# Performance work log

Hardware: AMD Instinct MI355X
Metric: run time of the kernel (lower is better)

The kernel has to match this reference:

```python
import jax, jax.numpy as jnp
import numpy as np

LN_EPS = 1e-5
BN_EPS = 1e-5


def setup_inputs() -> dict:
    key = jax.random.key(0)
    ks = jax.random.split(key, 16)
    N, C, T, H, W = 4, 256, 5, 28, 28
    Ci = 128
    CA = 128  # audio feature dim (hard-coded 128 in nn.Linear(128, in_channels))
    s = 0.02
    inp = {
        "x": jax.random.normal(ks[0], (N, C, T, H, W), jnp.float32),
        "audio": jax.random.normal(ks[1], (N, T, CA), jnp.float32),
        "align_W": jax.random.normal(ks[2], (C, CA), jnp.float32) * s,
        "align_b": jax.random.normal(ks[3], (C,), jnp.float32) * s,
        "g_W": jax.random.normal(ks[4], (Ci, C), jnp.float32) * s,
        "g_b": jax.random.normal(ks[5], (Ci,), jnp.float32) * s,
        "theta_W": jax.random.normal(ks[6], (Ci, C), jnp.float32) * s,
        "theta_b": jax.random.normal(ks[7], (Ci,), jnp.float32) * s,
        "phi_W": jax.random.normal(ks[8], (Ci, C), jnp.float32) * s,
        "phi_b": jax.random.normal(ks[9], (Ci,), jnp.float32) * s,
        "Wz_W": jax.random.normal(ks[10], (C, Ci), jnp.float32) * s,
        "Wz_b": jax.random.normal(ks[11], (C,), jnp.float32) * s,
        "bn_gamma": jax.random.normal(ks[12], (C,), jnp.float32) * s + 1.0,
        "bn_beta": jax.random.normal(ks[13], (C,), jnp.float32) * s,
        "bn_mean": jnp.zeros((C,), jnp.float32),
        "bn_var": jnp.ones((C,), jnp.float32),
        "ln_gamma": jnp.ones((C,), jnp.float32),
        "ln_beta": jnp.zeros((C,), jnp.float32),
    }
    return inp


def _tpavi(x, audio, align_W, align_b, g_W, g_b, theta_W, theta_b,
           phi_W, phi_b, Wz_W, Wz_b, bn_gamma, bn_beta, bn_mean, bn_var,
           ln_gamma, ln_beta):
    N, C, T, H, W = x.shape
    L = T * H * W
    # audio alignment: Linear(128 -> C), then broadcast over H, W
    audio_temp = jnp.einsum('ntc,oc->nto', audio, align_W) + align_b     # (N,T,C)
    a = audio_temp.transpose(0, 2, 1)[:, :, :, None, None]               # (N,C,T,1,1)
    a = jnp.broadcast_to(a, (N, C, T, H, W)).reshape(N, C, L)            # (N,C,L)

    xf = x.reshape(N, C, L)                                              # (N,C,L)
    # 1x1 conv3d == per-token channel mixing
    g_x = jnp.einsum('oc,ncl->nlo', g_W, xf) + g_b                       # (N,L,Ci)
    theta_x = jnp.einsum('oc,ncl->nlo', theta_W, xf) + theta_b           # (N,L,Ci)
    phi_x = jnp.einsum('oc,ncl->nol', phi_W, a) + phi_b[None, :, None]   # (N,Ci,L)

    # dot mode: f = theta phi^T, normalized by token count (no softmax)
    f = jnp.einsum('nlo,nok->nlk', theta_x, phi_x)                       # (N,L,L)
    f_div_C = f / L
    y = jnp.einsum('nlk,nko->nlo', f_div_C, g_x)                         # (N,L,Ci)

    y = y.transpose(0, 2, 1)                                             # (N,Ci,L)
    # W_z: 1x1 conv (Ci -> C) + BatchNorm3d (inference statistics)
    wy = jnp.einsum('oc,ncl->nol', Wz_W, y) + Wz_b[None, :, None]        # (N,C,L)
    inv = bn_gamma / jnp.sqrt(bn_var + BN_EPS)
    wy = (wy - bn_mean[None, :, None]) * inv[None, :, None] + bn_beta[None, :, None]

    z = wy.reshape(N, C, T, H, W) + x                                    # residual
    # LayerNorm over channel dim (channels-last in the original)
    zt = z.transpose(0, 2, 3, 4, 1)                                      # (N,T,H,W,C)
    mu = jnp.mean(zt, axis=-1, keepdims=True)
    var = jnp.mean(jnp.square(zt - mu), axis=-1, keepdims=True)
    zt = (zt - mu) / jnp.sqrt(var + LN_EPS) * ln_gamma + ln_beta
    z = zt.transpose(0, 4, 1, 2, 3)                                      # (N,C,T,H,W)
    return z, audio_temp


def reference(x, audio, align_W, align_b, g_W, g_b, theta_W, theta_b,
              phi_W, phi_b, Wz_W, Wz_b, bn_gamma, bn_beta, bn_mean, bn_var,
              ln_gamma, ln_beta):
    return _tpavi(x, audio, align_W, align_b, g_W, g_b, theta_W, theta_b,
                  phi_W, phi_b, Wz_W, Wz_b, bn_gamma, bn_beta, bn_mean, bn_var,
                  ln_gamma, ln_beta)
```

## Files before the change

### kernel.cpp

```cpp
#include <hip/hip_runtime.h>

#define N_DIM 4
#define C_DIM 256
#define T_DIM 5
#define HW    784
#define L_TOK 3920
#define CI    128
#define CA    128

#define WS_XS  0
#define WS_TP  5120
#define WS_GW  10240
#define WS_TB  15360

__global__ __launch_bounds__(256) void k1_xsum(const float* __restrict__ x,
                                               float* __restrict__ ws) {
    int bid = blockIdx.x;
    int n   = bid / (C_DIM * T_DIM);
    int rem = bid % (C_DIM * T_DIM);
    int c   = rem / T_DIM;
    int t   = rem % T_DIM;
    const float* base = x + ((size_t)(n * C_DIM + c) * T_DIM + t) * HW;
    int tid = threadIdx.x;

    float p = base[tid] + base[tid + 256] + base[tid + 512];
    if (tid < HW - 768) p += base[tid + 768];

    for (int off = 32; off > 0; off >>= 1) p += __shfl_down(p, off, 64);
    __shared__ float wsum[4];
    if ((tid & 63) == 0) wsum[tid >> 6] = p;
    __syncthreads();
    if (tid == 0) {
        ws[WS_XS + (n * T_DIM + t) * C_DIM + c] = wsum[0] + wsum[1] + wsum[2] + wsum[3];
    }
}

__global__ __launch_bounds__(256) void k2_small(
    const float* __restrict__ audio,   const float* __restrict__ align_W,
    const float* __restrict__ align_b, const float* __restrict__ g_W,
    const float* __restrict__ g_b,     const float* __restrict__ theta_W,
    const float* __restrict__ theta_b, const float* __restrict__ phi_W,
    const float* __restrict__ phi_b,   const float* __restrict__ Wz_W,
    const float* __restrict__ bn_gamma,const float* __restrict__ bn_var,
    float* __restrict__ ws, float* __restrict__ out_audio) {
    int nt = blockIdx.x;
    int tid = threadIdx.x;

    __shared__ float at_s[C_DIM];
    __shared__ float xs_s[C_DIM];
    __shared__ float phi_s[CI];
    __shared__ float g_s[CI];

    {
        const float* arow = audio + nt * CA;
        const float* wrow = align_W + tid * CA;
        float acc = align_b[tid];
        for (int a = 0; a < CA; ++a) acc = fmaf(arow[a], wrow[a], acc);
        at_s[tid] = acc;
        out_audio[nt * C_DIM + tid] = acc;
    }
    xs_s[tid] = ws[WS_XS + nt * C_DIM + tid];
    __syncthreads();

    if (tid < CI) {
        float acc = phi_b[tid];
        const float* wrow = phi_W + tid * C_DIM;
        for (int c = 0; c < C_DIM; ++c) acc = fmaf(wrow[c], at_s[c], acc);
        phi_s[tid] = acc;
        float ga = (float)HW * g_b[tid];
        const float* grow = g_W + tid * C_DIM;
        for (int c = 0; c < C_DIM; ++c) ga = fmaf(grow[c], xs_s[c], ga);
        g_s[tid] = ga;
    }
    __syncthreads();

    {
        float acc = 0.f;
        for (int o = 0; o < CI; ++o) acc = fmaf(theta_W[o * C_DIM + tid], phi_s[o], acc);
        ws[WS_TP + nt * C_DIM + tid] = acc;
    }
    if (tid == 0) {
        float acc = 0.f;
        for (int o = 0; o < CI; ++o) acc = fmaf(theta_b[o], phi_s[o], acc);
        ws[WS_TB + nt] = acc;
    }
    {
        float acc = 0.f;
        const float* wr = Wz_W + tid * CI;
        for (int o = 0; o < CI; ++o) acc = fmaf(wr[o], g_s[o], acc);
        float inv = bn_gamma[tid] * rsqrtf(bn_var[tid] + 1e-5f);
        ws[WS_GW + nt * C_DIM + tid] = acc * inv * (1.0f / (float)L_TOK);
    }
}

__global__ __launch_bounds__(256) void k3_main(
    const float* __restrict__ x,        const float* __restrict__ ws,
    const float* __restrict__ Wz_b,     const float* __restrict__ bn_gamma,
    const float* __restrict__ bn_beta,  const float* __restrict__ bn_mean,
    const float* __restrict__ bn_var,   const float* __restrict__ ln_gamma,
    const float* __restrict__ ln_beta,  float* __restrict__ out) {
    __shared__ float TPs[T_DIM * C_DIM];
    __shared__ float GWs[T_DIM * C_DIM];
    __shared__ float tb_s[T_DIM];
    __shared__ float B_s[C_DIM], lng_s[C_DIM], lnb_s[C_DIM];
    __shared__ float zbuf[64 * 257];
    __shared__ float Fp[256 * 5];
    __shared__ float Sp[256 * 2];

    int n    = blockIdx.y;
    int tile = blockIdx.x;
    int tid  = threadIdx.x;
    int g    = tid >> 6;
    int li   = tid & 63;
    int l    = tile * 64 + li;
    bool act = (l < L_TOK);

    for (int i = tid; i < T_DIM * C_DIM; i += 256) {
        TPs[i] = ws[WS_TP + n * T_DIM * C_DIM + i];
        GWs[i] = ws[WS_GW + n * T_DIM * C_DIM + i];
    }
    if (tid < T_DIM) tb_s[tid] = ws[WS_TB + n * T_DIM + tid];
    {
        int c = tid;
        float inv = bn_gamma[c] * rsqrtf(bn_var[c] + 1e-5f);
        B_s[c]   = (Wz_b[c] - bn_mean[c]) * inv + bn_beta[c];
        lng_s[c] = ln_gamma[c];
        lnb_s[c] = ln_beta[c];
    }
    __syncthreads();

    float F0 = 0, F1 = 0, F2 = 0, F3 = 0, F4 = 0;
    const float* xb = x + ((size_t)n * C_DIM + g * 64) * L_TOK + l;
    float* zrow = zbuf + li * 257 + g * 64;
    if (act) {
        for (int j = 0; j < 64; ++j) {
            float xv = xb[j * L_TOK];
            zrow[j] = xv;
            const float* tp = TPs + g * 64 + j;
            F0 = fmaf(xv, tp[0],    F0);
            F1 = fmaf(xv, tp[256],  F1);
            F2 = fmaf(xv, tp[512],  F2);
            F3 = fmaf(xv, tp[768],  F3);
            F4 = fmaf(xv, tp[1024], F4);
        }
    }
    Fp[tid * 5 + 0] = F0; Fp[tid * 5 + 1] = F1; Fp[tid * 5 + 2] = F2;
    Fp[tid * 5 + 3] = F3; Fp[tid * 5 + 4] = F4;
    __syncthreads();

    float Ft[T_DIM];
    #pragma unroll
    for (int t = 0; t < T_DIM; ++t)
        Ft[t] = Fp[(0 * 64 + li) * 5 + t] + Fp[(1 * 64 + li) * 5 + t] +
                Fp[(2 * 64 + li) * 5 + t] + Fp[(3 * 64 + li) * 5 + t] + tb_s[t];
    float s1 = 0.f, s2 = 0.f;
    for (int j = 0; j < 64; ++j) {
        int c = g * 64 + j;
        float zc = B_s[c] + zrow[j];
        zc = fmaf(Ft[0], GWs[c],        zc);
        zc = fmaf(Ft[1], GWs[256 + c],  zc);
        zc = fmaf(Ft[2], GWs[512 + c],  zc);
        zc = fmaf(Ft[3], GWs[768 + c],  zc);
        zc = fmaf(Ft[4], GWs[1024 + c], zc);
        zrow[j] = zc;
        s1 += zc;
        s2 = fmaf(zc, zc, s2);
    }
    Sp[tid * 2]     = s1;
    Sp[tid * 2 + 1] = s2;
    __syncthreads();

    float t1 = Sp[li * 2]     + Sp[(64 + li) * 2]     + Sp[(128 + li) * 2]     + Sp[(192 + li) * 2];
    float t2 = Sp[li * 2 + 1] + Sp[(64 + li) * 2 + 1] + Sp[(128 + li) * 2 + 1] + Sp[(192 + li) * 2 + 1];
    float mu   = t1 * (1.0f / C_DIM);
    float var  = t2 * (1.0f / C_DIM) - mu * mu;
    float rstd = rsqrtf(var + 1e-5f);
    if (act) {
        float* ob = out + ((size_t)n * C_DIM + g * 64) * L_TOK + l;
        for (int j = 0; j < 64; ++j) {
            int c = g * 64 + j;
            float zc = zrow[j];
            ob[j * L_TOK] = fmaf((zc - mu) * rstd, lng_s[c], lnb_s[c]);
        }
    }
}

extern "C" void kernel_launch(void* const* d_in, const int* in_sizes, int n_in,
                              void* d_out, int out_size, void* d_ws, size_t ws_size,
                              hipStream_t stream) {
    const float* x        = (const float*)d_in[0];
    const float* audio    = (const float*)d_in[1];
    const float* align_W  = (const float*)d_in[2];
    const float* align_b  = (const float*)d_in[3];
    const float* g_W      = (const float*)d_in[4];
    const float* g_b      = (const float*)d_in[5];
    const float* theta_W  = (const float*)d_in[6];
    const float* theta_b  = (const float*)d_in[7];
    const float* phi_W    = (const float*)d_in[8];
    const float* phi_b    = (const float*)d_in[9];
    const float* Wz_W     = (const float*)d_in[10];
    const float* Wz_b     = (const float*)d_in[11];
    const float* bn_gamma = (const float*)d_in[12];
    const float* bn_beta  = (const float*)d_in[13];
    const float* bn_mean  = (const float*)d_in[14];
    const float* bn_var   = (const float*)d_in[15];
    const float* ln_gamma = (const float*)d_in[16];
    const float* ln_beta  = (const float*)d_in[17];

    float* out       = (float*)d_out;
    float* out_audio = out + (size_t)N_DIM * C_DIM * L_TOK;
    float* ws        = (float*)d_ws;

    k1_xsum<<<N_DIM * C_DIM * T_DIM, 256, 0, stream>>>(x, ws);
    k2_small<<<N_DIM * T_DIM, 256, 0, stream>>>(
        audio, align_W, align_b, g_W, g_b, theta_W, theta_b, phi_W, phi_b,
        Wz_W, bn_gamma, bn_var, ws, out_audio);
    dim3 grid3((L_TOK + 63) / 64, N_DIM);
    k3_main<<<grid3, 256, 0, stream>>>(
        x, ws, Wz_b, bn_gamma, bn_beta, bn_mean, bn_var, ln_gamma, ln_beta, out);
}
```

Baseline: 138.6 us.

## Hold per-token channels in registers with 1024-thread blocks in main kernel

The main kernel now uses 1024 threads per block, with each wave covering 16 channels instead of 64. Each thread keeps its x values in registers, which removes the large shared-memory z buffer and the strided LDS traffic it caused. The partial-sum reductions widen to 16 waves. The x-sum and small projection kernels also switch to float4 loads with split accumulators, and the theta-bias dot product becomes a wave shuffle reduction. The gain in memory-level parallelism per token comes at the cost of heavier block-wide reductions and a larger block size.

```diff
diff --git a/kernel.cpp b/kernel.cpp
--- a/kernel.cpp
+++ b/kernel.cpp
@@ -20,12 +20,14 @@
     int rem = bid % (C_DIM * T_DIM);
     int c   = rem / T_DIM;
     int t   = rem % T_DIM;
-    const float* base = x + ((size_t)(n * C_DIM + c) * T_DIM + t) * HW;
+    const float4* base = (const float4*)(x + ((size_t)(n * C_DIM + c) * T_DIM + t) * HW);
     int tid = threadIdx.x;
 
-    float p = base[tid] + base[tid + 256] + base[tid + 512];
-    if (tid < HW - 768) p += base[tid + 768];
-
+    float p = 0.f;
+    if (tid < HW / 4) {
+        float4 v = base[tid];
+        p = (v.x + v.y) + (v.z + v.w);
+    }
     for (int off = 32; off > 0; off >>= 1) p += __shfl_down(p, off, 64);
     __shared__ float wsum[4];
     if ((tid & 63) == 0) wsum[tid >> 6] = p;
@@ -46,54 +48,89 @@
     int nt = blockIdx.x;
     int tid = threadIdx.x;
 
+    __shared__ float audio_s[CA];
     __shared__ float at_s[C_DIM];
     __shared__ float xs_s[C_DIM];
     __shared__ float phi_s[CI];
     __shared__ float g_s[CI];
 
+    if (tid < CA) audio_s[tid] = audio[nt * CA + tid];
+    xs_s[tid] = ws[WS_XS + nt * C_DIM + tid];
+    __syncthreads();
+
     {
-        const float* arow = audio + nt * CA;
-        const float* wrow = align_W + tid * CA;
-        float acc = align_b[tid];
-        for (int a = 0; a < CA; ++a) acc = fmaf(arow[a], wrow[a], acc);
+        const float4* row = (const float4*)(align_W + tid * CA);
+        float a0 = 0, a1 = 0, a2 = 0, a3 = 0;
+        #pragma unroll
+        for (int k = 0; k < CA / 4; ++k) {
+            float4 w = row[k];
+            a0 = fmaf(w.x, audio_s[4 * k + 0], a0);
+            a1 = fmaf(w.y, audio_s[4 * k + 1], a1);
+            a2 = fmaf(w.z, audio_s[4 * k + 2], a2);
+            a3 = fmaf(w.w, audio_s[4 * k + 3], a3);
+        }
+        float acc = align_b[tid] + (a0 + a1) + (a2 + a3);
         at_s[tid] = acc;
         out_audio[nt * C_DIM + tid] = acc;
     }
-    xs_s[tid] = ws[WS_XS + nt * C_DIM + tid];
     __syncthreads();
 
     if (tid < CI) {
-        float acc = phi_b[tid];
-        const float* wrow = phi_W + tid * C_DIM;
-        for (int c = 0; c < C_DIM; ++c) acc = fmaf(wrow[c], at_s[c], acc);
-        phi_s[tid] = acc;
-        float ga = (float)HW * g_b[tid];
-        const float* grow = g_W + tid * C_DIM;
-        for (int c = 0; c < C_DIM; ++c) ga = fmaf(grow[c], xs_s[c], ga);
-        g_s[tid] = ga;
+        const float4* prow = (const float4*)(phi_W + tid * C_DIM);
+        const float4* grow = (const float4*)(g_W + tid * C_DIM);
+        float p0 = 0, p1 = 0, p2 = 0, p3 = 0;
+        float q0 = 0, q1 = 0, q2 = 0, q3 = 0;
+        #pragma unroll
+        for (int k = 0; k < C_DIM / 4; ++k) {
+            float4 w = prow[k];
+            float4 u = grow[k];
+            float b0 = at_s[4 * k + 0], b1 = at_s[4 * k + 1];
+            float b2 = at_s[4 * k + 2], b3 = at_s[4 * k + 3];
+            float c0 = xs_s[4 * k + 0], c1 = xs_s[4 * k + 1];
+            float c2 = xs_s[4 * k + 2], c3 = xs_s[4 * k + 3];
+            p0 = fmaf(w.x, b0, p0); p1 = fmaf(w.y, b1, p1);
+            p2 = fmaf(w.z, b2, p2); p3 = fmaf(w.w, b3, p3);
+            q0 = fmaf(u.x, c0, q0); q1 = fmaf(u.y, c1, q1);
+            q2 = fmaf(u.z, c2, q2); q3 = fmaf(u.w, c3, q3);
+        }
+        phi_s[tid] = phi_b[tid] + (p0 + p1) + (p2 + p3);
+        g_s[tid]   = (float)HW * g_b[tid] + (q0 + q1) + (q2 + q3);
     }
     __syncthreads();
 
     {
-        float acc = 0.f;
-        for (int o = 0; o < CI; ++o) acc = fmaf(theta_W[o * C_DIM + tid], phi_s[o], acc);
-        ws[WS_TP + nt * C_DIM + tid] = acc;
-    }
-    if (tid == 0) {
-        float acc = 0.f;
-        for (int o = 0; o < CI; ++o) acc = fmaf(theta_b[o], phi_s[o], acc);
-        ws[WS_TB + nt] = acc;
+        float a0 = 0, a1 = 0, a2 = 0, a3 = 0;
+        #pragma unroll 4
+        for (int o = 0; o < CI; o += 4) {
+            a0 = fmaf(theta_W[(o + 0) * C_DIM + tid], phi_s[o + 0], a0);
+            a1 = fmaf(theta_W[(o + 1) * C_DIM + tid], phi_s[o + 1], a1);
+            a2 = fmaf(theta_W[(o + 2) * C_DIM + tid], phi_s[o + 2], a2);
+            a3 = fmaf(theta_W[(o + 3) * C_DIM + tid], phi_s[o + 3], a3);
+        }
+        ws[WS_TP + nt * C_DIM + tid] = (a0 + a1) + (a2 + a3);
+    }
+    if (tid < 64) {
+        float p = theta_b[tid] * phi_s[tid] + theta_b[tid + 64] * phi_s[tid + 64];
+        for (int off = 32; off > 0; off >>= 1) p += __shfl_down(p, off, 64);
+        if (tid == 0) ws[WS_TB + nt] = p;
     }
     {
-        float acc = 0.f;
-        const float* wr = Wz_W + tid * CI;
-        for (int o = 0; o < CI; ++o) acc = fmaf(wr[o], g_s[o], acc);
+        const float4* row = (const float4*)(Wz_W + tid * CI);
+        float a0 = 0, a1 = 0, a2 = 0, a3 = 0;
+        #pragma unroll
+        for (int k = 0; k < CI / 4; ++k) {
+            float4 w = row[k];
+            a0 = fmaf(w.x, g_s[4 * k + 0], a0);
+            a1 = fmaf(w.y, g_s[4 * k + 1], a1);
+            a2 = fmaf(w.z, g_s[4 * k + 2], a2);
+            a3 = fmaf(w.w, g_s[4 * k + 3], a3);
+        }
         float inv = bn_gamma[tid] * rsqrtf(bn_var[tid] + 1e-5f);
-        ws[WS_GW + nt * C_DIM + tid] = acc * inv * (1.0f / (float)L_TOK);
-    }
-}
-
-__global__ __launch_bounds__(256) void k3_main(
+        ws[WS_GW + nt * C_DIM + tid] = ((a0 + a1) + (a2 + a3)) * inv * (1.0f / (float)L_TOK);
+    }
+}
+
+__global__ __launch_bounds__(1024) void k3_main(
     const float* __restrict__ x,        const float* __restrict__ ws,
     const float* __restrict__ Wz_b,     const float* __restrict__ bn_gamma,
     const float* __restrict__ bn_beta,  const float* __restrict__ bn_mean,
@@ -103,9 +140,8 @@
     __shared__ float GWs[T_DIM * C_DIM];
     __shared__ float tb_s[T_DIM];
     __shared__ float B_s[C_DIM], lng_s[C_DIM], lnb_s[C_DIM];
-    __shared__ float zbuf[64 * 257];
-    __shared__ float Fp[256 * 5];
-    __shared__ float Sp[256 * 2];
+    __shared__ float Fp[T_DIM * 1024];
+    __shared__ float Sp[2 * 1024];
 
     int n    = blockIdx.y;
     int tile = blockIdx.x;
@@ -115,12 +151,12 @@
     int l    = tile * 64 + li;
     bool act = (l < L_TOK);
 
-    for (int i = tid; i < T_DIM * C_DIM; i += 256) {
+    for (int i = tid; i < T_DIM * C_DIM; i += 1024) {
         TPs[i] = ws[WS_TP + n * T_DIM * C_DIM + i];
         GWs[i] = ws[WS_GW + n * T_DIM * C_DIM + i];
     }
     if (tid < T_DIM) tb_s[tid] = ws[WS_TB + n * T_DIM + tid];
-    {
+    if (tid < C_DIM) {
         int c = tid;
         float inv = bn_gamma[c] * rsqrtf(bn_var[c] + 1e-5f);
         B_s[c]   = (Wz_b[c] - bn_mean[c]) * inv + bn_beta[c];
@@ -129,58 +165,66 @@
     }
     __syncthreads();
 
+    float xz[16];
+    const float* xb = x + ((size_t)(n * C_DIM + g * 16)) * L_TOK + l;
+    #pragma unroll
+    for (int j = 0; j < 16; ++j) xz[j] = act ? xb[(size_t)j * L_TOK] : 0.f;
+
     float F0 = 0, F1 = 0, F2 = 0, F3 = 0, F4 = 0;
-    const float* xb = x + ((size_t)n * C_DIM + g * 64) * L_TOK + l;
-    float* zrow = zbuf + li * 257 + g * 64;
-    if (act) {
-        for (int j = 0; j < 64; ++j) {
-            float xv = xb[j * L_TOK];
-            zrow[j] = xv;
-            const float* tp = TPs + g * 64 + j;
-            F0 = fmaf(xv, tp[0],    F0);
-            F1 = fmaf(xv, tp[256],  F1);
-            F2 = fmaf(xv, tp[512],  F2);
-            F3 = fmaf(xv, tp[768],  F3);
-            F4 = fmaf(xv, tp[1024], F4);
-        }
-    }
-    Fp[tid * 5 + 0] = F0; Fp[tid * 5 + 1] = F1; Fp[tid * 5 + 2] = F2;
-    Fp[tid * 5 + 3] = F3; Fp[tid * 5 + 4] = F4;
+    #pragma unroll
+    for (int j = 0; j < 16; ++j) {
+        const float* tp = TPs + g * 16 + j;
+        F0 = fmaf(xz[j], tp[0],    F0);
+        F1 = fmaf(xz[j], tp[256],  F1);
+        F2 = fmaf(xz[j], tp[512],  F2);
+        F3 = fmaf(xz[j], tp[768],  F3);
+        F4 = fmaf(xz[j], tp[1024], F4);
+    }
+    Fp[0 * 1024 + tid] = F0; Fp[1 * 1024 + tid] = F1; Fp[2 * 1024 + tid] = F2;
+    Fp[3 * 1024 + tid] = F3; Fp[4 * 1024 + tid] = F4;
     __syncthreads();
 
     float Ft[T_DIM];
     #pragma unroll
-    for (int t = 0; t < T_DIM; ++t)
-        Ft[t] = Fp[(0 * 64 + li) * 5 + t] + Fp[(1 * 64 + li) * 5 + t] +
-                Fp[(2 * 64 + li) * 5 + t] + Fp[(3 * 64 + li) * 5 + t] + tb_s[t];
+    for (int t = 0; t < T_DIM; ++t) {
+        float a = tb_s[t];
+        #pragma unroll
+        for (int w = 0; w < 16; ++w) a += Fp[t * 1024 + w * 64 + li];
+        Ft[t] = a;
+    }
     float s1 = 0.f, s2 = 0.f;
-    for (int j = 0; j < 64; ++j) {
-        int c = g * 64 + j;
-        float zc = B_s[c] + zrow[j];
+    #pragma unroll
+    for (int j = 0; j < 16; ++j) {
+        int c = g * 16 + j;
+        float zc = B_s[c] + xz[j];
         zc = fmaf(Ft[0], GWs[c],        zc);
         zc = fmaf(Ft[1], GWs[256 + c],  zc);
         zc = fmaf(Ft[2], GWs[512 + c],  zc);
         zc = fmaf(Ft[3], GWs[768 + c],  zc);
         zc = fmaf(Ft[4], GWs[1024 + c], zc);
-        zrow[j] = zc;
+        xz[j] = zc;
         s1 += zc;
         s2 = fmaf(zc, zc, s2);
     }
-    Sp[tid * 2]     = s1;
-    Sp[tid * 2 + 1] = s2;
-    __syncthreads();
-
-    float t1 = Sp[li * 2]     + Sp[(64 + li) * 2]     + Sp[(128 + li) * 2]     + Sp[(192 + li) * 2];
-    float t2 = Sp[li * 2 + 1] + Sp[(64 + li) * 2 + 1] + Sp[(128 + li) * 2 + 1] + Sp[(192 + li) * 2 + 1];
+    Sp[tid]        = s1;
+    Sp[1024 + tid] = s2;
+    __syncthreads();
+
+    float t1 = 0.f, t2 = 0.f;
+    #pragma unroll
+    for (int w = 0; w < 16; ++w) {
+        t1 += Sp[w * 64 + li];
+        t2 += Sp[1024 + w * 64 + li];
+    }
     float mu   = t1 * (1.0f / C_DIM);
     float var  = t2 * (1.0f / C_DIM) - mu * mu;
     float rstd = rsqrtf(var + 1e-5f);
     if (act) {
-        float* ob = out + ((size_t)n * C_DIM + g * 64) * L_TOK + l;
-        for (int j = 0; j < 64; ++j) {
-            int c = g * 64 + j;
-            float zc = zrow[j];
-            ob[j * L_TOK] = fmaf((zc - mu) * rstd, lng_s[c], lnb_s[c]);
+        float* ob = out + ((size_t)(n * C_DIM + g * 16)) * L_TOK + l;
+        #pragma unroll
+        for (int j = 0; j < 16; ++j) {
+            int c = g * 16 + j;
+            ob[(size_t)j * L_TOK] = fmaf((xz[j] - mu) * rstd, lng_s[c], lnb_s[c]);
         }
     }
 }
@@ -216,6 +260,6 @@
         audio, align_W, align_b, g_W, g_b, theta_W, theta_b, phi_W, phi_b,
         Wz_W, bn_gamma, bn_var, ws, out_audio);
     dim3 grid3((L_TOK + 63) / 64, N_DIM);
-    k3_main<<<grid3, 256, 0, stream>>>(
+    k3_main<<<grid3, 1024, 0, stream>>>(
         x, ws, Wz_b, bn_gamma, bn_beta, bn_mean, bn_var, ln_gamma, ln_beta, out);
 }
```

Result: no change. 136.0 us (-1.9%).
